# Optimization experiments

Hardware: AMD Instinct MI355X
Metric: run time of the kernel (lower is better)

The kernel has to match this reference:

```python
import jax, jax.numpy as jnp
import numpy as np

TAU = 0.2
NUM_SAMPLES = 8192
EMBED = 64


def setup_inputs() -> dict:
    key = jax.random.key(0)
    k1, k2, k3, k4 = jax.random.split(key, 4)
    all_users = jax.random.normal(k1, (100000, EMBED), dtype=jnp.float32)
    all_items = jax.random.normal(k2, (50000, EMBED), dtype=jnp.float32)
    user_index = jax.random.randint(k3, (NUM_SAMPLES,), 0, 100000, dtype=jnp.int64 if jax.config.jax_enable_x64 else jnp.int32)
    item_index = jax.random.randint(k4, (NUM_SAMPLES,), 0, 50000, dtype=jnp.int64 if jax.config.jax_enable_x64 else jnp.int32)
    return {"all_users": all_users, "all_items": all_items,
            "user_index": user_index, "item_index": item_index}


def _ssm_loss(embed, tau):
    # ratings: [N, N] similarity; positive is the diagonal (self-similarity).
    ratings = jnp.matmul(embed, embed.T) / tau            # [N, N]
    diag = jnp.sum(embed * embed, axis=1) / tau           # diag of embed@embed.T, no NxN gather
    # -log( exp(diag) / sum_j exp(ratings_ij) ) = logsumexp_row - diag
    lse = jax.scipy.special.logsumexp(ratings, axis=1)    # [N]
    return jnp.mean(lse - diag)


def reference(all_users, all_items, user_index, item_index):
    selected_users = all_users[user_index]                # [N, d]
    selected_items = all_items[item_index]                # [N, d]
    loss_u = _ssm_loss(selected_users, TAU)
    loss_i = _ssm_loss(selected_items, TAU)
    inv_loss = loss_u + loss_i
    return inv_loss, jnp.stack([loss_u, loss_i])
```

## Files before the change

kernel.cpp:

```cpp
#include <hip/hip_runtime.h>

#define EMBED        64
#define NS           8192
#define NTILE        256
#define JCHUNKS      8
#define JT_PER_CHUNK 32
#define C_L2E_TAU    7.21347520444482f

typedef _Float16 half8  __attribute__((ext_vector_type(8)));
typedef float    f32x16 __attribute__((ext_vector_type(16)));

#define GLDS16(g, l) __builtin_amdgcn_global_load_lds( \
    (const __attribute__((address_space(1))) void*)(g), \
    (__attribute__((address_space(3))) void*)(l), 16, 0, 0)

static __device__ __forceinline__ float exp2_raw(float x) {
  float r;
  asm("v_exp_f32 %0, %1" : "=v"(r) : "v"(x));
  return r;
}

__global__ __launch_bounds__(256) void prep_kernel(
    const float* __restrict__ users, const float* __restrict__ items,
    const int* __restrict__ uidx, const int* __restrict__ iidx,
    _Float16* __restrict__ Efrag, float* __restrict__ diag) {
  int b = blockIdx.x;
  int mat = b >> 8, tile = b & 255;
  int kt = threadIdx.x >> 6;
  int lane = threadIdx.x & 63;
  int r = lane & 31;
  int k0 = kt * 16 + (lane >> 5) * 8;
  int row = tile * 32 + r;
  int src = mat ? iidx[row] : uidx[row];
  const float4* basep =
      (const float4*)((mat ? items : users) + (size_t)src * EMBED + k0);
  float4 v0 = basep[0], v1 = basep[1];
  float vs[8] = {v0.x, v0.y, v0.z, v0.w, v1.x, v1.y, v1.z, v1.w};

  half8 hh, ll;
  float p = 0.f;
  #pragma unroll
  for (int j = 0; j < 8; ++j) {
    float v = vs[j];
    _Float16 h = (_Float16)v;
    hh[j] = h;
    ll[j] = (_Float16)(v - (float)h);
    p = fmaf(v, v, p);
  }
  _Float16* tb = Efrag + (size_t)(mat * NTILE + tile) * 4096;
  *(half8*)(tb + ((kt)     * 64 + lane) * 8) = hh;
  *(half8*)(tb + ((4 + kt) * 64 + lane) * 8) = ll;

  p += __shfl_xor(p, 32);
  __shared__ float ds[4][32];
  if (lane < 32) ds[kt][lane] = p;
  __syncthreads();
  if (threadIdx.x < 32)
    diag[mat * NS + tile * 32 + threadIdx.x] =
        ds[0][threadIdx.x] + ds[1][threadIdx.x] +
        ds[2][threadIdx.x] + ds[3][threadIdx.x];
}

__global__ __launch_bounds__(256) void ssm_mfma_kernel(
    const _Float16* __restrict__ Efrag, const float* __restrict__ diag,
    float* __restrict__ rowpart) {
  int b = blockIdx.x;
  int jc  = b & (JCHUNKS - 1);
  int rb  = (b >> 3) & 63;
  int mat = b >> 9;
  int wave = threadIdx.x >> 6;
  int lane = threadIdx.x & 63;
  int hf   = lane >> 5;

  int rowtile = rb * 4 + wave;
  int rowbase = rowtile * 32;
  const _Float16* Em = Efrag + (size_t)mat * NTILE * 4096;

  half8 a[8];
  #pragma unroll
  for (int f = 0; f < 8; ++f)
    a[f] = *(const half8*)(Em + (size_t)rowtile * 4096 + (f * 64 + lane) * 8);

  float negdv[16];
  #pragma unroll
  for (int r = 0; r < 16; ++r)
    negdv[r] = -diag[mat * NS + rowbase + (r & 3) + 8 * (r >> 2) + 4 * hf];

  float rs[16];
  #pragma unroll
  for (int r = 0; r < 16; ++r) rs[r] = 0.f;

  __shared__ __align__(16) _Float16 Bbuf[2][4096];

  int jt0 = jc * JT_PER_CHUNK;
  auto stage = [&](int buf, int jt) {
    const char* src = (const char*)(Em + (size_t)(jt0 + jt) * 4096) + wave * 2048;
    char* dst = (char*)&Bbuf[buf][0] + wave * 2048;
    GLDS16(src + lane * 16, dst);
    GLDS16(src + 1024 + lane * 16, dst + 1024);
  };

  stage(0, 0);
  __syncthreads();

  for (int jt = 0; jt < JT_PER_CHUNK; ++jt) {
    int cur = jt & 1;
    if (jt + 1 < JT_PER_CHUNK) stage(cur ^ 1, jt + 1);

    half8 bh[4], bl[4];
    #pragma unroll
    for (int k = 0; k < 4; ++k) {
      bh[k] = *(const half8*)(&Bbuf[cur][0] + ((k)     * 64 + lane) * 8);
      bl[k] = *(const half8*)(&Bbuf[cur][0] + ((4 + k) * 64 + lane) * 8);
    }

    f32x16 acc;
    #pragma unroll
    for (int r = 0; r < 16; ++r) acc[r] = negdv[r];

    #pragma unroll
    for (int k = 0; k < 4; ++k)
      acc = __builtin_amdgcn_mfma_f32_32x32x16_f16(a[k], bh[k], acc, 0, 0, 0);
    #pragma unroll
    for (int k = 0; k < 4; ++k)
      acc = __builtin_amdgcn_mfma_f32_32x32x16_f16(a[k], bl[k], acc, 0, 0, 0);
    #pragma unroll
    for (int k = 0; k < 4; ++k)
      acc = __builtin_amdgcn_mfma_f32_32x32x16_f16(a[4 + k], bh[k], acc, 0, 0, 0);

    #pragma unroll
    for (int r = 0; r < 16; ++r)
      rs[r] += exp2_raw(acc[r] * C_L2E_TAU);

    __syncthreads();
  }

  #pragma unroll
  for (int r = 0; r < 16; ++r) {
    float v = rs[r];
    v += __shfl_xor(v, 16);
    v += __shfl_xor(v, 8);
    v += __shfl_xor(v, 4);
    v += __shfl_xor(v, 2);
    v += __shfl_xor(v, 1);
    if ((lane & 31) == 0)
      rowpart[jc * (2 * NS) + mat * NS + rowbase +
              (r & 3) + 8 * (r >> 2) + 4 * hf] = v;
  }
}

__global__ __launch_bounds__(256) void fin1_kernel(
    const float* __restrict__ rowpart, float* __restrict__ partial) {
  int r = blockIdx.x * 256 + threadIdx.x;
  float s = 0.f;
  #pragma unroll
  for (int c = 0; c < JCHUNKS; ++c) s += rowpart[c * (2 * NS) + r];
  float l = logf(s);
  #pragma unroll
  for (int off = 32; off; off >>= 1) l += __shfl_down(l, off);
  __shared__ float ps[4];
  if ((threadIdx.x & 63) == 0) ps[threadIdx.x >> 6] = l;
  __syncthreads();
  if (threadIdx.x == 0) partial[blockIdx.x] = ps[0] + ps[1] + ps[2] + ps[3];
}

__global__ __launch_bounds__(64) void fin2_kernel(
    const float* __restrict__ partial, float* __restrict__ out) {
  int t = threadIdx.x;
  float v = partial[t];
  float vu = (t < 32) ? v : 0.f;
  float vi = (t < 32) ? 0.f : v;
  #pragma unroll
  for (int off = 32; off; off >>= 1) {
    vu += __shfl_down(vu, off);
    vi += __shfl_down(vi, off);
  }
  if (t == 0) {
    float su = vu * (1.0f / NS);
    float si = vi * (1.0f / NS);
    out[0] = su + si;
    out[1] = su;
    out[2] = si;
  }
}

extern "C" void kernel_launch(void* const* d_in, const int* in_sizes, int n_in,
                              void* d_out, int out_size, void* d_ws, size_t ws_size,
                              hipStream_t stream) {
  const float* users = (const float*)d_in[0];
  const float* items = (const float*)d_in[1];
  const int*   uidx  = (const int*)d_in[2];
  const int*   iidx  = (const int*)d_in[3];
  float* out = (float*)d_out;

  _Float16* Efrag = (_Float16*)d_ws;
  float* diag     = (float*)((char*)d_ws + (size_t)4194304);
  float* rowpart  = diag + 2 * NS;
  float* partial  = (float*)d_ws;

  prep_kernel<<<2 * NTILE, 256, 0, stream>>>(users, items, uidx, iidx, Efrag, diag);
  ssm_mfma_kernel<<<2 * 64 * JCHUNKS, 256, 0, stream>>>(Efrag, diag, rowpart);
  fin1_kernel<<<64, 256, 0, stream>>>(rowpart, partial);
  fin2_kernel<<<1, 64, 0, stream>>>(partial, out);
}
```

Baseline: 135.6 us.

## Compute two row tiles per wave, load B from global into registers, merge finalize kernels

```diff
diff --git a/kernel.cpp b/kernel.cpp
--- a/kernel.cpp
+++ b/kernel.cpp
@@ -9,10 +9,6 @@
 
 typedef _Float16 half8  __attribute__((ext_vector_type(8)));
 typedef float    f32x16 __attribute__((ext_vector_type(16)));
-
-#define GLDS16(g, l) __builtin_amdgcn_global_load_lds( \
-    (const __attribute__((address_space(1))) void*)(g), \
-    (__attribute__((address_space(3))) void*)(l), 16, 0, 0)
 
 static __device__ __forceinline__ float exp2_raw(float x) {
   float r;
@@ -61,123 +57,132 @@
         ds[2][threadIdx.x] + ds[3][threadIdx.x];
 }
 
-__global__ __launch_bounds__(256) void ssm_mfma_kernel(
+__global__ __launch_bounds__(256, 2) void ssm_mfma_kernel(
     const _Float16* __restrict__ Efrag, const float* __restrict__ diag,
     float* __restrict__ rowpart) {
   int b = blockIdx.x;
   int jc  = b & (JCHUNKS - 1);
-  int rb  = (b >> 3) & 63;
-  int mat = b >> 9;
+  int sg  = (b >> 3) & 31;
+  int mat = b >> 8;
   int wave = threadIdx.x >> 6;
   int lane = threadIdx.x & 63;
   int hf   = lane >> 5;
 
-  int rowtile = rb * 4 + wave;
-  int rowbase = rowtile * 32;
+  int strip = sg * 4 + wave;
+  int rt0 = strip * 2, rt1 = rt0 + 1;
   const _Float16* Em = Efrag + (size_t)mat * NTILE * 4096;
 
-  half8 a[8];
-  #pragma unroll
-  for (int f = 0; f < 8; ++f)
-    a[f] = *(const half8*)(Em + (size_t)rowtile * 4096 + (f * 64 + lane) * 8);
-
-  float negdv[16];
-  #pragma unroll
-  for (int r = 0; r < 16; ++r)
-    negdv[r] = -diag[mat * NS + rowbase + (r & 3) + 8 * (r >> 2) + 4 * hf];
-
-  float rs[16];
-  #pragma unroll
-  for (int r = 0; r < 16; ++r) rs[r] = 0.f;
-
-  __shared__ __align__(16) _Float16 Bbuf[2][4096];
-
-  int jt0 = jc * JT_PER_CHUNK;
-  auto stage = [&](int buf, int jt) {
-    const char* src = (const char*)(Em + (size_t)(jt0 + jt) * 4096) + wave * 2048;
-    char* dst = (char*)&Bbuf[buf][0] + wave * 2048;
-    GLDS16(src + lane * 16, dst);
-    GLDS16(src + 1024 + lane * 16, dst + 1024);
+  half8 a0[8], a1[8];
+  #pragma unroll
+  for (int f = 0; f < 8; ++f) {
+    a0[f] = *(const half8*)(Em + (size_t)rt0 * 4096 + (f * 64 + lane) * 8);
+    a1[f] = *(const half8*)(Em + (size_t)rt1 * 4096 + (f * 64 + lane) * 8);
+  }
+
+  float negdv0[16], negdv1[16];
+  #pragma unroll
+  for (int r = 0; r < 16; ++r) {
+    int rl = (r & 3) + 8 * (r >> 2) + 4 * hf;
+    negdv0[r] = -diag[mat * NS + rt0 * 32 + rl];
+    negdv1[r] = -diag[mat * NS + rt1 * 32 + rl];
+  }
+
+  float rs0[16], rs1[16];
+  #pragma unroll
+  for (int r = 0; r < 16; ++r) { rs0[r] = 0.f; rs1[r] = 0.f; }
+
+  int tj0 = jc * JT_PER_CHUNK;
+
+  auto loadB = [&](int tj, half8* bb) {
+    const _Float16* B = Em + (size_t)tj * 4096;
+    #pragma unroll
+    for (int f = 0; f < 8; ++f)
+      bb[f] = *(const half8*)(B + (f * 64 + lane) * 8);
   };
-
-  stage(0, 0);
+  auto compute = [&](const half8* bb) {
+    f32x16 acc;
+    #pragma unroll
+    for (int r = 0; r < 16; ++r) acc[r] = negdv0[r];
+    #pragma unroll
+    for (int k = 0; k < 4; ++k)
+      acc = __builtin_amdgcn_mfma_f32_32x32x16_f16(a0[k], bb[k], acc, 0, 0, 0);
+    #pragma unroll
+    for (int k = 0; k < 4; ++k)
+      acc = __builtin_amdgcn_mfma_f32_32x32x16_f16(a0[k], bb[4 + k], acc, 0, 0, 0);
+    #pragma unroll
+    for (int k = 0; k < 4; ++k)
+      acc = __builtin_amdgcn_mfma_f32_32x32x16_f16(a0[4 + k], bb[k], acc, 0, 0, 0);
+    #pragma unroll
+    for (int r = 0; r < 16; ++r)
+      rs0[r] += exp2_raw(acc[r] * C_L2E_TAU);
+
+    #pragma unroll
+    for (int r = 0; r < 16; ++r) acc[r] = negdv1[r];
+    #pragma unroll
+    for (int k = 0; k < 4; ++k)
+      acc = __builtin_amdgcn_mfma_f32_32x32x16_f16(a1[k], bb[k], acc, 0, 0, 0);
+    #pragma unroll
+    for (int k = 0; k < 4; ++k)
+      acc = __builtin_amdgcn_mfma_f32_32x32x16_f16(a1[k], bb[4 + k], acc, 0, 0, 0);
+    #pragma unroll
+    for (int k = 0; k < 4; ++k)
+      acc = __builtin_amdgcn_mfma_f32_32x32x16_f16(a1[4 + k], bb[k], acc, 0, 0, 0);
+    #pragma unroll
+    for (int r = 0; r < 16; ++r)
+      rs1[r] += exp2_raw(acc[r] * C_L2E_TAU);
+  };
+
+  half8 bA[8], bB[8];
+  loadB(tj0, bA);
+  #pragma unroll 1
+  for (int jt = 0; jt < JT_PER_CHUNK; jt += 2) {
+    loadB(tj0 + jt + 1, bB);
+    compute(bA);
+    if (jt + 2 < JT_PER_CHUNK) loadB(tj0 + jt + 2, bA);
+    compute(bB);
+  }
+
+  #pragma unroll
+  for (int r = 0; r < 16; ++r) {
+    float v0 = rs0[r], v1 = rs1[r];
+    #pragma unroll
+    for (int off = 16; off; off >>= 1) {
+      v0 += __shfl_xor(v0, off);
+      v1 += __shfl_xor(v1, off);
+    }
+    if ((lane & 31) == 0) {
+      int rl = (r & 3) + 8 * (r >> 2) + 4 * hf;
+      rowpart[jc * (2 * NS) + mat * NS + rt0 * 32 + rl] = v0;
+      rowpart[jc * (2 * NS) + mat * NS + rt1 * 32 + rl] = v1;
+    }
+  }
+}
+
+__global__ __launch_bounds__(1024) void finalize_kernel(
+    const float* __restrict__ rowpart, float* __restrict__ out) {
+  float lu = 0.f, li = 0.f;
+  for (int r = threadIdx.x; r < 2 * NS; r += 1024) {
+    float s = 0.f;
+    #pragma unroll
+    for (int c = 0; c < JCHUNKS; ++c) s += rowpart[c * (2 * NS) + r];
+    float l = logf(s);
+    if (r < NS) lu += l; else li += l;
+  }
+  #pragma unroll
+  for (int off = 32; off; off >>= 1) {
+    lu += __shfl_down(lu, off);
+    li += __shfl_down(li, off);
+  }
+  __shared__ float red[2][16];
+  int wave = threadIdx.x >> 6;
+  if ((threadIdx.x & 63) == 0) { red[0][wave] = lu; red[1][wave] = li; }
   __syncthreads();
-
-  for (int jt = 0; jt < JT_PER_CHUNK; ++jt) {
-    int cur = jt & 1;
-    if (jt + 1 < JT_PER_CHUNK) stage(cur ^ 1, jt + 1);
-
-    half8 bh[4], bl[4];
-    #pragma unroll
-    for (int k = 0; k < 4; ++k) {
-      bh[k] = *(const half8*)(&Bbuf[cur][0] + ((k)     * 64 + lane) * 8);
-      bl[k] = *(const half8*)(&Bbuf[cur][0] + ((4 + k) * 64 + lane) * 8);
-    }
-
-    f32x16 acc;
-    #pragma unroll
-    for (int r = 0; r < 16; ++r) acc[r] = negdv[r];
-
-    #pragma unroll
-    for (int k = 0; k < 4; ++k)
-      acc = __builtin_amdgcn_mfma_f32_32x32x16_f16(a[k], bh[k], acc, 0, 0, 0);
-    #pragma unroll
-    for (int k = 0; k < 4; ++k)
-      acc = __builtin_amdgcn_mfma_f32_32x32x16_f16(a[k], bl[k], acc, 0, 0, 0);
-    #pragma unroll
-    for (int k = 0; k < 4; ++k)
-      acc = __builtin_amdgcn_mfma_f32_32x32x16_f16(a[4 + k], bh[k], acc, 0, 0, 0);
-
-    #pragma unroll
-    for (int r = 0; r < 16; ++r)
-      rs[r] += exp2_raw(acc[r] * C_L2E_TAU);
-
-    __syncthreads();
-  }
-
-  #pragma unroll
-  for (int r = 0; r < 16; ++r) {
-    float v = rs[r];
-    v += __shfl_xor(v, 16);
-    v += __shfl_xor(v, 8);
-    v += __shfl_xor(v, 4);
-    v += __shfl_xor(v, 2);
-    v += __shfl_xor(v, 1);
-    if ((lane & 31) == 0)
-      rowpart[jc * (2 * NS) + mat * NS + rowbase +
-              (r & 3) + 8 * (r >> 2) + 4 * hf] = v;
-  }
-}
-
-__global__ __launch_bounds__(256) void fin1_kernel(
-    const float* __restrict__ rowpart, float* __restrict__ partial) {
-  int r = blockIdx.x * 256 + threadIdx.x;
-  float s = 0.f;
-  #pragma unroll
-  for (int c = 0; c < JCHUNKS; ++c) s += rowpart[c * (2 * NS) + r];
-  float l = logf(s);
-  #pragma unroll
-  for (int off = 32; off; off >>= 1) l += __shfl_down(l, off);
-  __shared__ float ps[4];
-  if ((threadIdx.x & 63) == 0) ps[threadIdx.x >> 6] = l;
-  __syncthreads();
-  if (threadIdx.x == 0) partial[blockIdx.x] = ps[0] + ps[1] + ps[2] + ps[3];
-}
-
-__global__ __launch_bounds__(64) void fin2_kernel(
-    const float* __restrict__ partial, float* __restrict__ out) {
-  int t = threadIdx.x;
-  float v = partial[t];
-  float vu = (t < 32) ? v : 0.f;
-  float vi = (t < 32) ? 0.f : v;
-  #pragma unroll
-  for (int off = 32; off; off >>= 1) {
-    vu += __shfl_down(vu, off);
-    vi += __shfl_down(vi, off);
-  }
-  if (t == 0) {
-    float su = vu * (1.0f / NS);
-    float si = vi * (1.0f / NS);
+  if (threadIdx.x == 0) {
+    float su = 0.f, si = 0.f;
+    #pragma unroll
+    for (int w = 0; w < 16; ++w) { su += red[0][w]; si += red[1][w]; }
+    su *= (1.0f / NS);
+    si *= (1.0f / NS);
     out[0] = su + si;
     out[1] = su;
     out[2] = si;
@@ -196,10 +201,8 @@
   _Float16* Efrag = (_Float16*)d_ws;
   float* diag     = (float*)((char*)d_ws + (size_t)4194304);
   float* rowpart  = diag + 2 * NS;
-  float* partial  = (float*)d_ws;
 
   prep_kernel<<<2 * NTILE, 256, 0, stream>>>(users, items, uidx, iidx, Efrag, diag);
-  ssm_mfma_kernel<<<2 * 64 * JCHUNKS, 256, 0, stream>>>(Efrag, diag, rowpart);
-  fin1_kernel<<<64, 256, 0, stream>>>(rowpart, partial);
-  fin2_kernel<<<1, 64, 0, stream>>>(partial, out);
-}
+  ssm_mfma_kernel<<<2 * 32 * JCHUNKS, 256, 0, stream>>>(Efrag, diag, rowpart);
+  finalize_kernel<<<1, 1024, 0, stream>>>(rowpart, out);
+}
```

Measured after the change: 140.4 us. 1.04x slower.

## Load B fragments directly from global, drop LDS staging, merge finalize kernels

Applied to the files above, without the earlier changes.

```diff
diff --git a/kernel.cpp b/kernel.cpp
--- a/kernel.cpp
+++ b/kernel.cpp
@@ -9,10 +9,6 @@
 
 typedef _Float16 half8  __attribute__((ext_vector_type(8)));
 typedef float    f32x16 __attribute__((ext_vector_type(16)));
-
-#define GLDS16(g, l) __builtin_amdgcn_global_load_lds( \
-    (const __attribute__((address_space(1))) void*)(g), \
-    (__attribute__((address_space(3))) void*)(l), 16, 0, 0)
 
 static __device__ __forceinline__ float exp2_raw(float x) {
   float r;
@@ -61,19 +57,18 @@
         ds[2][threadIdx.x] + ds[3][threadIdx.x];
 }
 
-__global__ __launch_bounds__(256) void ssm_mfma_kernel(
+__global__ __launch_bounds__(256, 4) void ssm_mfma_kernel(
     const _Float16* __restrict__ Efrag, const float* __restrict__ diag,
     float* __restrict__ rowpart) {
   int b = blockIdx.x;
   int jc  = b & (JCHUNKS - 1);
-  int rb  = (b >> 3) & 63;
+  int sg  = (b >> 3) & 63;
   int mat = b >> 9;
   int wave = threadIdx.x >> 6;
   int lane = threadIdx.x & 63;
   int hf   = lane >> 5;
 
-  int rowtile = rb * 4 + wave;
-  int rowbase = rowtile * 32;
+  int rowtile = sg * 4 + wave;
   const _Float16* Em = Efrag + (size_t)mat * NTILE * 4096;
 
   half8 a[8];
@@ -84,35 +79,24 @@
   float negdv[16];
   #pragma unroll
   for (int r = 0; r < 16; ++r)
-    negdv[r] = -diag[mat * NS + rowbase + (r & 3) + 8 * (r >> 2) + 4 * hf];
+    negdv[r] = -diag[mat * NS + rowtile * 32 + (r & 3) + 8 * (r >> 2) + 4 * hf];
 
   float rs[16];
   #pragma unroll
   for (int r = 0; r < 16; ++r) rs[r] = 0.f;
 
-  __shared__ __align__(16) _Float16 Bbuf[2][4096];
+  int tj0 = jc * JT_PER_CHUNK;
 
-  int jt0 = jc * JT_PER_CHUNK;
-  auto stage = [&](int buf, int jt) {
-    const char* src = (const char*)(Em + (size_t)(jt0 + jt) * 4096) + wave * 2048;
-    char* dst = (char*)&Bbuf[buf][0] + wave * 2048;
-    GLDS16(src + lane * 16, dst);
-    GLDS16(src + 1024 + lane * 16, dst + 1024);
-  };
-
-  stage(0, 0);
-  __syncthreads();
-
+  #pragma unroll 2
   for (int jt = 0; jt < JT_PER_CHUNK; ++jt) {
-    int cur = jt & 1;
-    if (jt + 1 < JT_PER_CHUNK) stage(cur ^ 1, jt + 1);
-
+    const _Float16* B = Em + (size_t)(tj0 + jt) * 4096;
     half8 bh[4], bl[4];
     #pragma unroll
-    for (int k = 0; k < 4; ++k) {
-      bh[k] = *(const half8*)(&Bbuf[cur][0] + ((k)     * 64 + lane) * 8);
-      bl[k] = *(const half8*)(&Bbuf[cur][0] + ((4 + k) * 64 + lane) * 8);
-    }
+    for (int k = 0; k < 4; ++k)
+      bh[k] = *(const half8*)(B + ((k)     * 64 + lane) * 8);
+    #pragma unroll
+    for (int k = 0; k < 4; ++k)
+      bl[k] = *(const half8*)(B + ((4 + k) * 64 + lane) * 8);
 
     f32x16 acc;
     #pragma unroll
@@ -131,53 +115,44 @@
     #pragma unroll
     for (int r = 0; r < 16; ++r)
       rs[r] += exp2_raw(acc[r] * C_L2E_TAU);
-
-    __syncthreads();
   }
 
   #pragma unroll
   for (int r = 0; r < 16; ++r) {
     float v = rs[r];
-    v += __shfl_xor(v, 16);
-    v += __shfl_xor(v, 8);
-    v += __shfl_xor(v, 4);
-    v += __shfl_xor(v, 2);
-    v += __shfl_xor(v, 1);
+    #pragma unroll
+    for (int off = 16; off; off >>= 1) v += __shfl_xor(v, off);
     if ((lane & 31) == 0)
-      rowpart[jc * (2 * NS) + mat * NS + rowbase +
+      rowpart[jc * (2 * NS) + mat * NS + rowtile * 32 +
               (r & 3) + 8 * (r >> 2) + 4 * hf] = v;
   }
 }
 
-__global__ __launch_bounds__(256) void fin1_kernel(
-    const float* __restrict__ rowpart, float* __restrict__ partial) {
-  int r = blockIdx.x * 256 + threadIdx.x;
-  float s = 0.f;
-  #pragma unroll
-  for (int c = 0; c < JCHUNKS; ++c) s += rowpart[c * (2 * NS) + r];
-  float l = logf(s);
-  #pragma unroll
-  for (int off = 32; off; off >>= 1) l += __shfl_down(l, off);
-  __shared__ float ps[4];
-  if ((threadIdx.x & 63) == 0) ps[threadIdx.x >> 6] = l;
-  __syncthreads();
-  if (threadIdx.x == 0) partial[blockIdx.x] = ps[0] + ps[1] + ps[2] + ps[3];
-}
-
-__global__ __launch_bounds__(64) void fin2_kernel(
-    const float* __restrict__ partial, float* __restrict__ out) {
-  int t = threadIdx.x;
-  float v = partial[t];
-  float vu = (t < 32) ? v : 0.f;
-  float vi = (t < 32) ? 0.f : v;
+__global__ __launch_bounds__(1024) void finalize_kernel(
+    const float* __restrict__ rowpart, float* __restrict__ out) {
+  float lu = 0.f, li = 0.f;
+  for (int r = threadIdx.x; r < 2 * NS; r += 1024) {
+    float s = 0.f;
+    #pragma unroll
+    for (int c = 0; c < JCHUNKS; ++c) s += rowpart[c * (2 * NS) + r];
+    float l = logf(s);
+    if (r < NS) lu += l; else li += l;
+  }
   #pragma unroll
   for (int off = 32; off; off >>= 1) {
-    vu += __shfl_down(vu, off);
-    vi += __shfl_down(vi, off);
+    lu += __shfl_down(lu, off);
+    li += __shfl_down(li, off);
   }
-  if (t == 0) {
-    float su = vu * (1.0f / NS);
-    float si = vi * (1.0f / NS);
+  __shared__ float red[2][16];
+  int wave = threadIdx.x >> 6;
+  if ((threadIdx.x & 63) == 0) { red[0][wave] = lu; red[1][wave] = li; }
+  __syncthreads();
+  if (threadIdx.x == 0) {
+    float su = 0.f, si = 0.f;
+    #pragma unroll
+    for (int w = 0; w < 16; ++w) { su += red[0][w]; si += red[1][w]; }
+    su *= (1.0f / NS);
+    si *= (1.0f / NS);
     out[0] = su + si;
     out[1] = su;
     out[2] = si;
@@ -196,10 +171,8 @@
   _Float16* Efrag = (_Float16*)d_ws;
   float* diag     = (float*)((char*)d_ws + (size_t)4194304);
   float* rowpart  = diag + 2 * NS;
-  float* partial  = (float*)d_ws;
 
   prep_kernel<<<2 * NTILE, 256, 0, stream>>>(users, items, uidx, iidx, Efrag, diag);
   ssm_mfma_kernel<<<2 * 64 * JCHUNKS, 256, 0, stream>>>(Efrag, diag, rowpart);
-  fin1_kernel<<<64, 256, 0, stream>>>(rowpart, partial);
-  fin2_kernel<<<1, 64, 0, stream>>>(partial, out);
+  finalize_kernel<<<1, 1024, 0, stream>>>(rowpart, out);
 }
```

Result: slower. 146.3 us (+7.8%).
